# Kernel tuning notes

Measured on AMD Instinct MI355X. Metric: run time of the kernel, lower is better.

## Reference

```python
import jax, jax.numpy as jnp
import numpy as np

QB = 127.0  # act_bits=8 -> 2**(8-1)-1
EPS = 1e-5


def _ste(x, q):
    # straight-through estimator: forward = q, backward = identity
    return x + jax.lax.stop_gradient(q - x)


def bitlinear(x, W, b):
    """BitNet-b1.58 linear: ternary weights (per-tensor mean-abs scale),
    8-bit per-token absmax activations, dequantized matmul + bias."""
    w_scale = jnp.clip(jnp.mean(jnp.abs(W)), EPS, None)
    Wq = _ste(W, jnp.clip(jnp.round(W / w_scale), -1.0, 1.0) * w_scale)  # ternary * scale
    x_scale = jnp.clip(jnp.max(jnp.abs(x), axis=-1, keepdims=True), EPS, None)
    xq = _ste(x, jnp.clip(jnp.round(x * (QB / x_scale)), -QB - 1.0, QB) * (x_scale / QB))
    # x: [B, N, d_in], W: [d_out, d_in] -> [B, N, d_out]
    return jnp.einsum('bnd,hd->bnh', xq, Wq) + b


def setup_inputs() -> dict:
    key = jax.random.key(0)
    k0, k1, k2 = jax.random.split(key, 3)
    B, N, D = 8, 4096, 1024
    H = int(D * 4.0)
    x = jax.random.normal(k0, (B, N, D), dtype=jnp.float32)
    W1 = jax.random.normal(k1, (H, D), dtype=jnp.float32) * 0.02
    b1 = jnp.zeros((H,), dtype=jnp.float32)
    W2 = jax.random.normal(k2, (D, H), dtype=jnp.float32) * 0.02
    b2 = jnp.zeros((D,), dtype=jnp.float32)
    return {"x": x, "W1": W1, "b1": b1, "W2": W2, "b2": b2}


def reference(x, W1, b1, W2, b2):
    h = bitlinear(x, W1, b1)                 # [B, N, H]
    h = jax.nn.gelu(h, approximate=False)    # torch nn.GELU default = exact erf
    # dropout with p=0.0 is identity
    return bitlinear(h, W2, b2)              # [B, N, D]
```

## Files before the change

kernel.cpp:

```cpp
#include <hip/hip_runtime.h>
#include <hip/hip_bf16.h>
#include <math.h>


typedef int int32x4 __attribute__((ext_vector_type(4)));

typedef const void __attribute__((address_space(1))) gv_t;
typedef void __attribute__((address_space(3))) lv_t;

__device__ __forceinline__ void gload_lds16(const signed char* g,
                                            signed char* l) {
  __builtin_amdgcn_global_load_lds((gv_t*)g, (lv_t*)l, 16, 0, 0);
}

__device__ __forceinline__ float gelu_erf(float v) {
  return 0.5f * v * (1.0f + erff(v * 0.70710678118654752440f));
}

__device__ __forceinline__ unsigned short bf16_rne(float v) {
  unsigned u = __float_as_uint(v);
  u += 0x7fffu + ((u >> 16) & 1u);
  return (unsigned short)(u >> 16);
}

__device__ __forceinline__ void store4(float* p, const float o[4]) {
  float4 t; t.x = o[0]; t.y = o[1]; t.z = o[2]; t.w = o[3];
  *(float4*)p = t;
}
__device__ __forceinline__ void store4(__hip_bfloat16* p, const float o[4]) {
  ushort4 t;
  t.x = bf16_rne(o[0]); t.y = bf16_rne(o[1]);
  t.z = bf16_rne(o[2]); t.w = bf16_rne(o[3]);
  *(ushort4*)p = t;
}

__device__ __forceinline__ void load4v(const float* p, float v[4]) {
  const float4 t = *(const float4*)p;
  v[0] = t.x; v[1] = t.y; v[2] = t.z; v[3] = t.w;
}
__device__ __forceinline__ void load4v(const __hip_bfloat16* p, float v[4]) {
  const ushort4 t = *(const ushort4*)p;
  v[0] = __uint_as_float((unsigned)t.x << 16);
  v[1] = __uint_as_float((unsigned)t.y << 16);
  v[2] = __uint_as_float((unsigned)t.z << 16);
  v[3] = __uint_as_float((unsigned)t.w << 16);
}

__global__ __launch_bounds__(256) void absmean_partial(
    const float* __restrict__ W, double* __restrict__ part) {
  const int tid = threadIdx.x;
  const long base = (long)blockIdx.x * 8192;
  double s = 0.0;
#pragma unroll
  for (int c = 0; c < 8; ++c) {
    const float4 v = *(const float4*)&W[base + c * 1024 + tid * 4];
    s += (double)fabsf(v.x) + (double)fabsf(v.y) +
         (double)fabsf(v.z) + (double)fabsf(v.w);
  }
  __shared__ double sm[256];
  sm[tid] = s; __syncthreads();
  for (int off = 128; off; off >>= 1) {
    if (tid < off) sm[tid] += sm[tid + off];
    __syncthreads();
  }
  if (tid == 0) part[blockIdx.x] = sm[0];
}

__global__ __launch_bounds__(256) void absmean_final(
    const double* __restrict__ part, double* __restrict__ out, double n) {
  const int tid = threadIdx.x;
  __shared__ double sm[256];
  sm[tid] = part[tid] + part[tid + 256];
  __syncthreads();
  for (int off = 128; off; off >>= 1) {
    if (tid < off) sm[tid] += sm[tid + off];
    __syncthreads();
  }
  if (tid == 0) out[0] = fmax(sm[0] / n, 1e-5);
}

__global__ __launch_bounds__(256) void quant_w(
    const float* __restrict__ W, const double* __restrict__ wsP,
    signed char* __restrict__ Wq) {
  const double ws = *wsP;
  const long i = ((long)blockIdx.x * 256 + threadIdx.x) * 4;
  const float4 v = *(const float4*)&W[i];
  const float vv[4] = {v.x, v.y, v.z, v.w};
  int pack = 0;
#pragma unroll
  for (int q = 0; q < 4; ++q) {
    double r = rint((double)vv[q] / ws);
    r = fmin(fmax(r, -1.0), 1.0);
    pack |= (((int)r) & 0xff) << (8 * q);
  }
  *(int*)&Wq[i] = pack;
}

template <int L, bool GELU, typename GT>
__global__ __launch_bounds__(256) void quant_rows(
    const GT* __restrict__ X, signed char* __restrict__ Xq,
    float* __restrict__ dsc) {
  constexpr int CH = L / 1024;
  const long row = blockIdx.x;
  const int tid = threadIdx.x;
  const GT* xr = X + row * (long)L;
  float v[CH][4];
  float m = 0.f;
#pragma unroll
  for (int c = 0; c < CH; ++c) {
    load4v(xr + c * 1024 + tid * 4, v[c]);
#pragma unroll
    for (int q = 0; q < 4; ++q) {
      if (GELU) v[c][q] = gelu_erf(v[c][q]);
      m = fmaxf(m, fabsf(v[c][q]));
    }
  }
#pragma unroll
  for (int off = 32; off; off >>= 1) m = fmaxf(m, __shfl_down(m, off, 64));
  __shared__ float wmx[4];
  if ((tid & 63) == 0) wmx[tid >> 6] = m;
  __syncthreads();
  float ms = fmaxf(fmaxf(wmx[0], wmx[1]), fmaxf(wmx[2], wmx[3]));
  ms = fmaxf(ms, 1e-5f);
  const double inv = 127.0 / (double)ms;
#pragma unroll
  for (int c = 0; c < CH; ++c) {
    int pack = 0;
#pragma unroll
    for (int q = 0; q < 4; ++q) {
      double r = rint((double)v[c][q] * inv);
      r = fmin(fmax(r, -128.0), 127.0);
      pack |= (((int)r) & 0xff) << (8 * q);
    }
    *(int*)&Xq[row * (long)L + c * 1024 + tid * 4] = pack;
  }
  if (tid == 0) dsc[row] = (float)((double)ms / 127.0);
}

template <typename GT>
__global__ __launch_bounds__(512, 2) void gemm_i8_ls(
    const signed char* __restrict__ A, const signed char* __restrict__ Bm,
    const float* __restrict__ dA, const double* __restrict__ wsB,
    const float* __restrict__ bias, GT* __restrict__ C,
    int K, int Ncol, int nx) {
  __shared__ signed char LDS[131072];
  const int tid = threadIdx.x;
  const int lane = tid & 63;
  const int wave = tid >> 6;
  const int wm = wave >> 2;
  const int wn = wave & 3;

  const int cpx = gridDim.x >> 3;
  const int wg = ((int)blockIdx.x & 7) * cpx + ((int)blockIdx.x >> 3);
  const long rowBase = (long)(wg / nx) * 256;
  const long colBase = (long)(wg % nx) * 256;
  const int NT = K >> 7;

  const int dd = tid << 4;
  const int srow = dd >> 7;
  const int scol = (dd & 127) ^ ((srow & 7) << 4);
  const long k64 = 64L * K;
  const signed char* sA0 = A + (rowBase + srow) * (long)K + scol;
  const signed char* sB0 = Bm + (colBase + srow) * (long)K + scol;

  auto STAGE_A2 = [&](int t, int h) {
    const signed char* p = sA0 + ((long)t << 7) + (2 * h) * k64;
    signed char* l = &LDS[((t & 1) << 15) + dd + h * 16384];
    gload_lds16(p, l);
    gload_lds16(p + k64, l + 8192);
  };
  auto STAGE_B4 = [&](int t) {
    const signed char* p = sB0 + ((long)t << 7);
    signed char* l = &LDS[65536 + ((t & 1) << 15) + dd];
#pragma unroll
    for (int i = 0; i < 4; ++i) gload_lds16(p + i * k64, l + i * 8192);
  };

  const int rl = lane & 15;
  const int col0 = (((lane >> 4) << 4)) ^ ((rl & 7) << 4);
  const int aRow = wm * 16384 + rl * 128;
  const int bRow = wn * 8192 + rl * 128;

  int32x4 acc[8][4] = {};

  STAGE_B4(0);
  STAGE_A2(0, 0); STAGE_A2(0, 1);
  STAGE_B4(1);

  for (int t = 0; t < NT; ++t) {
    if (t + 1 < NT) asm volatile("s_waitcnt vmcnt(4)" ::: "memory");
    else            asm volatile("s_waitcnt vmcnt(0)" ::: "memory");
    __builtin_amdgcn_s_barrier();

    const signed char* At = &LDS[(t & 1) << 15];
    const signed char* Bt = &LDS[65536 + ((t & 1) << 15)];
    int32x4 af[4], bf[4];

    auto LDA = [&](int mih, int kc6) {
#pragma unroll
      for (int i = 0; i < 4; ++i)
        af[i] = *(const int32x4*)(At + aRow + (mih * 4 + i) * 2048 +
                                  (col0 ^ kc6));
    };
    auto LDB = [&](int kc6) {
#pragma unroll
      for (int nj = 0; nj < 4; ++nj)
        bf[nj] = *(const int32x4*)(Bt + bRow + nj * 2048 + (col0 ^ kc6));
    };
    auto MFMA16 = [&](int mih) {
      __builtin_amdgcn_s_setprio(1);
#pragma unroll
      for (int i = 0; i < 4; ++i)
#pragma unroll
        for (int nj = 0; nj < 4; ++nj)
          acc[mih * 4 + i][nj] = __builtin_amdgcn_mfma_i32_16x16x64_i8(
              bf[nj], af[i], acc[mih * 4 + i][nj], 0, 0, 0);
      __builtin_amdgcn_s_setprio(0);
    };

    LDB(0);
    LDA(0, 0);
    if (t + 1 < NT) STAGE_A2(t + 1, 0);
    MFMA16(0);
    LDA(1, 0);
    if (t + 1 < NT) STAGE_A2(t + 1, 1);
    MFMA16(1);
    LDB(64);
    LDA(0, 64);
    MFMA16(0);
    asm volatile("s_waitcnt lgkmcnt(0)" ::: "memory");
    __builtin_amdgcn_s_barrier();
    LDA(1, 64);
    if (t + 2 < NT) STAGE_B4(t + 2);
    MFMA16(1);
  }

  const double wsd = *wsB;
  const int rq4 = (lane >> 4) << 2;
  float sc[8];
#pragma unroll
  for (int mi = 0; mi < 8; ++mi)
    sc[mi] = (float)((double)dA[rowBase + wm * 128 + mi * 16 + rl] * wsd);
  float4 bv[4];
#pragma unroll
  for (int nj = 0; nj < 4; ++nj)
    bv[nj] = *(const float4*)&bias[colBase + wn * 64 + nj * 16 + rq4];
#pragma unroll
  for (int mi = 0; mi < 8; ++mi) {
    const long row = rowBase + wm * 128 + mi * 16 + rl;
    GT* crow = C + row * (long)Ncol + colBase + wn * 64 + rq4;
#pragma unroll
    for (int nj = 0; nj < 4; ++nj) {
      float o[4];
      o[0] = (float)acc[mi][nj][0] * sc[mi] + bv[nj].x;
      o[1] = (float)acc[mi][nj][1] * sc[mi] + bv[nj].y;
      o[2] = (float)acc[mi][nj][2] * sc[mi] + bv[nj].z;
      o[3] = (float)acc[mi][nj][3] * sc[mi] + bv[nj].w;
      store4(&crow[nj * 16], o);
    }
  }
}

extern "C" void kernel_launch(void* const* d_in, const int* in_sizes, int n_in,
                              void* d_out, int out_size, void* d_ws,
                              size_t ws_size, hipStream_t stream) {
  const float* x  = (const float*)d_in[0];
  const float* W1 = (const float*)d_in[1];
  const float* b1 = (const float*)d_in[2];
  const float* W2 = (const float*)d_in[3];
  const float* b2 = (const float*)d_in[4];
  const int D = in_sizes[4];
  const int H = in_sizes[2];
  const long M = (long)in_sizes[0] / D;
  float* out = (float*)d_out;

  if (D != 1024 || H != 4096 || (M % 256) != 0) return;

  char* wsp = (char*)d_ws;
  size_t off = 0;
  auto alloc = [&](size_t bytes) {
    void* p = wsp + off;
    off = (off + bytes + 255) & ~(size_t)255;
    return p;
  };
  signed char* wq1 = (signed char*)alloc((size_t)H * D);
  signed char* wq2 = (signed char*)alloc((size_t)D * H);
  signed char* xq  = (signed char*)alloc((size_t)M * D);
  signed char* gq  = (signed char*)alloc((size_t)M * H);
  float* dx = (float*)alloc((size_t)M * 4);
  float* dg = (float*)alloc((size_t)M * 4);
  double* part = (double*)alloc(512 * 8);
  double* ws1 = (double*)alloc(8);
  double* ws2 = (double*)alloc(8);
  __hip_bfloat16* h = (__hip_bfloat16*)alloc((size_t)M * H * 2);
  if (off > ws_size) return;

  const long nW = (long)H * D;
  absmean_partial<<<nW / 8192, 256, 0, stream>>>(W1, part);
  absmean_final<<<1, 256, 0, stream>>>(part, ws1, (double)nW);
  absmean_partial<<<nW / 8192, 256, 0, stream>>>(W2, part);
  absmean_final<<<1, 256, 0, stream>>>(part, ws2, (double)nW);
  quant_w<<<nW / 1024, 256, 0, stream>>>(W1, ws1, wq1);
  quant_w<<<nW / 1024, 256, 0, stream>>>(W2, ws2, wq2);
  quant_rows<1024, false, float><<<M, 256, 0, stream>>>(x, xq, dx);

  const int g1 = (H / 256) * (int)(M / 256);
  const int g2 = (D / 256) * (int)(M / 256);
  gemm_i8_ls<__hip_bfloat16><<<g1, 512, 0, stream>>>(
      xq, wq1, dx, ws1, b1, h, D, H, H / 256);
  quant_rows<4096, true, __hip_bfloat16><<<M, 256, 0, stream>>>(h, gq, dg);
  gemm_i8_ls<float><<<g2, 512, 0, stream>>>(
      gq, wq2, dg, ws2, b2, out, H, D, D / 256);
}
```

Before: 467.7 us.

## Switch int8 GEMM to 32x32x32 MFMA tiles with double-buffered fragments

Replaces the 16x16x64 int8 MFMA with 32x32x32 int8 MFMA, so each wave covers its 128x64 tile with 4x2 larger accumulators. It also reorders LDS fragment loads into two ping-pong register sets, adding barriers between phases. The larger MFMA needs fewer LDS fragment loads per unit of math and fewer instructions. The epilogue is rewritten for the 32x32 output layout, and the extra barriers and register pressure may limit the gain.

```diff
diff --git a/kernel.cpp b/kernel.cpp
--- a/kernel.cpp
+++ b/kernel.cpp
@@ -4,6 +4,7 @@
 
 
 typedef int int32x4 __attribute__((ext_vector_type(4)));
+typedef int int32x16 __attribute__((ext_vector_type(16)));
 
 typedef const void __attribute__((address_space(1))) gv_t;
 typedef void __attribute__((address_space(3))) lv_t;
@@ -138,7 +139,7 @@
 }
 
 template <typename GT>
-__global__ __launch_bounds__(512, 2) void gemm_i8_ls(
+__global__ __launch_bounds__(512, 2) void gemm_i8_32(
     const signed char* __restrict__ A, const signed char* __restrict__ Bm,
     const float* __restrict__ dA, const double* __restrict__ wsB,
     const float* __restrict__ bias, GT* __restrict__ C,
@@ -176,12 +177,19 @@
     for (int i = 0; i < 4; ++i) gload_lds16(p + i * k64, l + i * 8192);
   };
 
-  const int rl = lane & 15;
-  const int col0 = (((lane >> 4) << 4)) ^ ((rl & 7) << 4);
-  const int aRow = wm * 16384 + rl * 128;
-  const int bRow = wn * 8192 + rl * 128;
-
-  int32x4 acc[8][4] = {};
+  const int ml = lane & 31;
+  const int h16 = (lane >> 5) << 4;
+  const int xm = (lane & 7) << 4;
+  int rA[4], rB[2], colX[4];
+#pragma unroll
+  for (int tm = 0; tm < 4; ++tm) rA[tm] = (wm * 128 + tm * 32 + ml) * 128;
+#pragma unroll
+  for (int tn = 0; tn < 2; ++tn) rB[tn] = (wn * 64 + tn * 32 + ml) * 128;
+#pragma unroll
+  for (int s = 0; s < 4; ++s) colX[s] = ((s << 5) + h16) ^ xm;
+
+  int32x16 acc[4][2] = {};
+  int32x4 afA[4], bfA[2], afB[4], bfB[2];
 
   STAGE_B4(0);
   STAGE_A2(0, 0); STAGE_A2(0, 1);
@@ -194,69 +202,77 @@
 
     const signed char* At = &LDS[(t & 1) << 15];
     const signed char* Bt = &LDS[65536 + ((t & 1) << 15)];
-    int32x4 af[4], bf[4];
-
-    auto LDA = [&](int mih, int kc6) {
-#pragma unroll
-      for (int i = 0; i < 4; ++i)
-        af[i] = *(const int32x4*)(At + aRow + (mih * 4 + i) * 2048 +
-                                  (col0 ^ kc6));
+
+    auto LDF = [&](int32x4 af[4], int32x4 bf[2], int s) {
+#pragma unroll
+      for (int tn = 0; tn < 2; ++tn)
+        bf[tn] = *(const int32x4*)(Bt + rB[tn] + colX[s]);
+#pragma unroll
+      for (int tm = 0; tm < 4; ++tm)
+        af[tm] = *(const int32x4*)(At + rA[tm] + colX[s]);
     };
-    auto LDB = [&](int kc6) {
-#pragma unroll
-      for (int nj = 0; nj < 4; ++nj)
-        bf[nj] = *(const int32x4*)(Bt + bRow + nj * 2048 + (col0 ^ kc6));
-    };
-    auto MFMA16 = [&](int mih) {
+    auto MFMA8 = [&](int32x4 af[4], int32x4 bf[2]) {
       __builtin_amdgcn_s_setprio(1);
 #pragma unroll
-      for (int i = 0; i < 4; ++i)
-#pragma unroll
-        for (int nj = 0; nj < 4; ++nj)
-          acc[mih * 4 + i][nj] = __builtin_amdgcn_mfma_i32_16x16x64_i8(
-              bf[nj], af[i], acc[mih * 4 + i][nj], 0, 0, 0);
+      for (int tm = 0; tm < 4; ++tm)
+#pragma unroll
+        for (int tn = 0; tn < 2; ++tn)
+          acc[tm][tn] = __builtin_amdgcn_mfma_i32_32x32x32_i8(
+              bf[tn], af[tm], acc[tm][tn], 0, 0, 0);
       __builtin_amdgcn_s_setprio(0);
     };
 
-    LDB(0);
-    LDA(0, 0);
+    LDF(afA, bfA, 0);
+    LDF(afB, bfB, 1);
     if (t + 1 < NT) STAGE_A2(t + 1, 0);
-    MFMA16(0);
-    LDA(1, 0);
+    __builtin_amdgcn_s_barrier();
+    MFMA8(afA, bfA);
+
+    LDF(afA, bfA, 2);
     if (t + 1 < NT) STAGE_A2(t + 1, 1);
-    MFMA16(1);
-    LDB(64);
-    LDA(0, 64);
-    MFMA16(0);
+    __builtin_amdgcn_s_barrier();
+    MFMA8(afB, bfB);
+
+    LDF(afB, bfB, 3);
+    __builtin_amdgcn_s_barrier();
+    MFMA8(afA, bfA);
+
     asm volatile("s_waitcnt lgkmcnt(0)" ::: "memory");
     __builtin_amdgcn_s_barrier();
-    LDA(1, 64);
     if (t + 2 < NT) STAGE_B4(t + 2);
-    MFMA16(1);
+    MFMA8(afB, bfB);
   }
 
   const double wsd = *wsB;
-  const int rq4 = (lane >> 4) << 2;
-  float sc[8];
-#pragma unroll
-  for (int mi = 0; mi < 8; ++mi)
-    sc[mi] = (float)((double)dA[rowBase + wm * 128 + mi * 16 + rl] * wsd);
-  float4 bv[4];
-#pragma unroll
-  for (int nj = 0; nj < 4; ++nj)
-    bv[nj] = *(const float4*)&bias[colBase + wn * 64 + nj * 16 + rq4];
-#pragma unroll
-  for (int mi = 0; mi < 8; ++mi) {
-    const long row = rowBase + wm * 128 + mi * 16 + rl;
-    GT* crow = C + row * (long)Ncol + colBase + wn * 64 + rq4;
-#pragma unroll
-    for (int nj = 0; nj < 4; ++nj) {
-      float o[4];
-      o[0] = (float)acc[mi][nj][0] * sc[mi] + bv[nj].x;
-      o[1] = (float)acc[mi][nj][1] * sc[mi] + bv[nj].y;
-      o[2] = (float)acc[mi][nj][2] * sc[mi] + bv[nj].z;
-      o[3] = (float)acc[mi][nj][3] * sc[mi] + bv[nj].w;
-      store4(&crow[nj * 16], o);
+  const int h5 = (lane >> 5) << 2;
+  float sc[4];
+#pragma unroll
+  for (int tm = 0; tm < 4; ++tm)
+    sc[tm] = (float)((double)dA[rowBase + wm * 128 + tm * 32 + ml] * wsd);
+  float4 bv[2][4];
+#pragma unroll
+  for (int tn = 0; tn < 2; ++tn)
+#pragma unroll
+    for (int rq = 0; rq < 4; ++rq)
+      bv[tn][rq] =
+          *(const float4*)&bias[colBase + wn * 64 + tn * 32 + h5 + rq * 8];
+#pragma unroll
+  for (int tm = 0; tm < 4; ++tm) {
+    const long row = rowBase + wm * 128 + tm * 32 + ml;
+    GT* crow = C + row * (long)Ncol + colBase + wn * 64 + h5;
+#pragma unroll
+    for (int tn = 0; tn < 2; ++tn) {
+#pragma unroll
+      for (int rq = 0; rq < 4; ++rq) {
+        float o[4];
+#pragma unroll
+        for (int j = 0; j < 4; ++j) {
+          const float bj = (j == 0) ? bv[tn][rq].x : (j == 1) ? bv[tn][rq].y
+                           : (j == 2) ? bv[tn][rq].z : bv[tn][rq].w;
+          o[j] = (float)acc[tm][tn][rq * 4 + j] * sc[tm] + bj;
+        }
+        store4(&crow[tn * 32 + rq * 8], o);
+      }
     }
   }
 }
@@ -306,9 +322,9 @@
 
   const int g1 = (H / 256) * (int)(M / 256);
   const int g2 = (D / 256) * (int)(M / 256);
-  gemm_i8_ls<__hip_bfloat16><<<g1, 512, 0, stream>>>(
+  gemm_i8_32<__hip_bfloat16><<<g1, 512, 0, stream>>>(
       xq, wq1, dx, ws1, b1, h, D, H, H / 256);
   quant_rows<4096, true, __hip_bfloat16><<<M, 256, 0, stream>>>(h, gq, dg);
-  gemm_i8_ls<float><<<g2, 512, 0, stream>>>(
+  gemm_i8_32<float><<<g2, 512, 0, stream>>>(
       gq, wq2, dg, ws2, b2, out, H, D, D / 256);
 }
```

After: 524.9 us. 12.2% more time.
